# Performance work log

Measured on AMD Instinct MI355X. Metric: run time of the kernel, lower is better.

Reference implementation:

```python
import jax, jax.numpy as jnp
import numpy as np

N_NODES = 100000
N_EDGES = 1600000
IN_DIM = 64
HIDDEN_DIM = 64


def setup_inputs() -> dict:
    key = jax.random.key(0)
    ks = jax.random.split(key, 8)
    x = jax.random.normal(ks[0], (N_NODES, IN_DIM), dtype=jnp.float32)
    edge_index = jax.random.randint(ks[1], (2, N_EDGES), 0, N_NODES, dtype=jnp.int32)
    s = 1.0 / np.sqrt(IN_DIM)
    sh = 1.0 / np.sqrt(HIDDEN_DIM)
    # SAGEConv params: lin_l (applied to mean-aggregated neighbors, with bias),
    # lin_r (applied to root/self features, no bias) -- PyG defaults.
    w1l = jax.random.uniform(ks[2], (IN_DIM, HIDDEN_DIM), jnp.float32, -s, s)
    b1l = jax.random.uniform(ks[3], (HIDDEN_DIM,), jnp.float32, -s, s)
    w1r = jax.random.uniform(ks[4], (IN_DIM, HIDDEN_DIM), jnp.float32, -s, s)
    w2l = jax.random.uniform(ks[5], (HIDDEN_DIM, HIDDEN_DIM), jnp.float32, -sh, sh)
    b2l = jax.random.uniform(ks[6], (HIDDEN_DIM,), jnp.float32, -sh, sh)
    w2r = jax.random.uniform(ks[7], (HIDDEN_DIM, HIDDEN_DIM), jnp.float32, -sh, sh)
    return {"x": x, "edge_index": edge_index, "w1l": w1l, "b1l": b1l,
            "w1r": w1r, "w2l": w2l, "b2l": b2l, "w2r": w2r}


def reference(x, edge_index, w1l, b1l, w1r, w2l, b2l, w2r):
    n = x.shape[0]
    src, dst = edge_index[0], edge_index[1]
    # in-degree (number of incoming messages per target node), clamped to 1
    deg = jax.ops.segment_sum(jnp.ones(src.shape, x.dtype), dst, num_segments=n)
    inv_deg = 1.0 / jnp.maximum(deg, 1.0)  # [N]

    def sage_conv(h, wl, bl, wr):
        # mean aggregation of neighbor messages: scatter-add then normalize
        agg = jax.ops.segment_sum(h[src], dst, num_segments=n) * inv_deg[:, None]
        return agg @ wl + bl + h @ wr

    h = jax.nn.relu(sage_conv(x, w1l, b1l, w1r))  # conv1 + relu
    return sage_conv(h, w2l, b2l, w2r)            # conv2 (no activation)
```

## Files before the change

kernel.cpp:

```cpp
#include <hip/hip_runtime.h>
#include <hip/hip_fp16.h>


#define DIM 64
#define BN 64
#define MAXBUCK 2048
#define CHUNK 4096
#define GCAP 2048
#define WT_STRIDE 72

using f16x8 = __attribute__((ext_vector_type(8))) _Float16;
using f32x4 = __attribute__((ext_vector_type(4))) float;

__device__ inline void addh8(float* acc, float4 raw) {
    const __half2* hp = (const __half2*)&raw;
#pragma unroll
    for (int k = 0; k < 4; ++k) {
        float2 f = __half22float2(hp[k]);
        acc[2 * k]     += f.x;
        acc[2 * k + 1] += f.y;
    }
}

__global__ __launch_bounds__(256) void prehist_kernel(const int* __restrict__ dst,
                                                      int* __restrict__ ghist,
                                                      int nE, int nbuck) {
    __shared__ int hist[MAXBUCK];
    const int t = threadIdx.x;
    for (int k = t; k < nbuck; k += 256) hist[k] = 0;
    __syncthreads();
    const int base = blockIdx.x * CHUNK;
    const int end = min(nE, base + CHUNK);
    for (int i = base + t; i < end; i += 256)
        atomicAdd(&hist[dst[i] >> 6], 1);
    __syncthreads();
    for (int k = t; k < nbuck; k += 256)
        if (hist[k]) atomicAdd(&ghist[k], hist[k]);
}

__global__ __launch_bounds__(1024) void scan_kernel(const int* __restrict__ ghist,
                                                    int* __restrict__ boff,
                                                    int* __restrict__ gcur, int nbuck) {
    __shared__ int sa[2048], sb[2048];
    const int t = threadIdx.x;
    int v0 = (t < nbuck) ? ghist[t] : 0;
    int v1 = (t + 1024 < nbuck) ? ghist[t + 1024] : 0;
    sa[t] = v0; sa[t + 1024] = v1;
    __syncthreads();
    int* in = sa; int* out = sb;
    for (int d = 1; d < 2048; d <<= 1) {
        out[t] = in[t] + ((t >= d) ? in[t - d] : 0);
        int i2 = t + 1024;
        out[i2] = in[i2] + ((i2 >= d) ? in[i2 - d] : 0);
        __syncthreads();
        int* tmp = in; in = out; out = tmp;
    }
    if (t < nbuck) { int e = in[t] - v0; boff[t] = e; gcur[t] = e; }
    if (t + 1024 < nbuck) { int e = in[t + 1024] - v1; boff[t + 1024] = e; gcur[t + 1024] = e; }
    if (t == 0) boff[nbuck] = in[2047];
}

__device__ inline void load_bfrag(const float* __restrict__ H, long long nn, int lq,
                                  f16x8& b0, f16x8& b1) {
    const float* p = &H[nn * 64 + lq * 8];
    float4 u0 = *(const float4*)p;
    float4 u1 = *(const float4*)(p + 4);
    float4 u2 = *(const float4*)(p + 32);
    float4 u3 = *(const float4*)(p + 36);
    b0[0] = (_Float16)u0.x; b0[1] = (_Float16)u0.y; b0[2] = (_Float16)u0.z; b0[3] = (_Float16)u0.w;
    b0[4] = (_Float16)u1.x; b0[5] = (_Float16)u1.y; b0[6] = (_Float16)u1.z; b0[7] = (_Float16)u1.w;
    b1[0] = (_Float16)u2.x; b1[1] = (_Float16)u2.y; b1[2] = (_Float16)u2.z; b1[3] = (_Float16)u2.w;
    b1[4] = (_Float16)u3.x; b1[5] = (_Float16)u3.y; b1[6] = (_Float16)u3.z; b1[7] = (_Float16)u3.w;
}

__device__ void gemm_body(int bid, __half* wt,
                          const float* __restrict__ H,
                          const float* __restrict__ Wl, const float* __restrict__ Wr,
                          const float* __restrict__ bias,
                          __half* __restrict__ A, __half* __restrict__ Dbuf, int n) {
    const int t = threadIdx.x;
    for (int i = t; i < 4096; i += 256) {
        int k = i >> 6, m = i & 63;
        wt[(size_t)m * WT_STRIDE + k] = __float2half(Wl[i]);
        wt[(size_t)(64 + m) * WT_STRIDE + k] = __float2half(Wr[i]);
    }
    __syncthreads();
    const int lane = t & 63, wave = t >> 6;
    const int ln = lane & 15, lq = lane >> 4;
    f16x8 af[2][4][2];
#pragma unroll
    for (int mat = 0; mat < 2; ++mat)
#pragma unroll
        for (int mt = 0; mt < 4; ++mt)
#pragma unroll
            for (int ki = 0; ki < 2; ++ki)
                af[mat][mt][ki] = *(const f16x8*)&wt[(size_t)(mat * 64 + mt * 16 + ln) * WT_STRIDE
                                                     + ki * 32 + lq * 8];
    float4 bf[4];
#pragma unroll
    for (int mt = 0; mt < 4; ++mt)
        bf[mt] = *(const float4*)&bias[mt * 16 + lq * 4];

    const int base = bid * 256;
    for (int it = 0; it < 4; ++it) {
        const int node = base + it * 64 + wave * 16 + ln;
        const long long nn = (node < n) ? node : (n - 1);
        f16x8 b0, b1;
        load_bfrag(H, nn, lq, b0, b1);
        f32x4 acc[2][4];
#pragma unroll
        for (int mat = 0; mat < 2; ++mat)
#pragma unroll
            for (int mt = 0; mt < 4; ++mt) {
                f32x4 z = {0.f, 0.f, 0.f, 0.f};
                z = __builtin_amdgcn_mfma_f32_16x16x32_f16(af[mat][mt][0], b0, z, 0, 0, 0);
                z = __builtin_amdgcn_mfma_f32_16x16x32_f16(af[mat][mt][1], b1, z, 0, 0, 0);
                acc[mat][mt] = z;
            }
        if (node < n) {
#pragma unroll
            for (int mt = 0; mt < 4; ++mt) {
                union { __half2 h[2]; float2 f; } u;
                u.h[0] = __floats2half2_rn(acc[0][mt][0], acc[0][mt][1]);
                u.h[1] = __floats2half2_rn(acc[0][mt][2], acc[0][mt][3]);
                *(float2*)&A[(size_t)node * 64 + mt * 16 + lq * 4] = u.f;
                union { __half2 h[2]; float2 f; } v;
                v.h[0] = __floats2half2_rn(acc[1][mt][0] + bf[mt].x, acc[1][mt][1] + bf[mt].y);
                v.h[1] = __floats2half2_rn(acc[1][mt][2] + bf[mt].z, acc[1][mt][3] + bf[mt].w);
                *(float2*)&Dbuf[(size_t)node * 64 + mt * 16 + lq * 4] = v.f;
            }
        }
    }
}

__global__ __launch_bounds__(256) void part_gemm_kernel(const int* __restrict__ src,
                                                        const int* __restrict__ dst,
                                                        int* __restrict__ gcur,
                                                        unsigned* __restrict__ P,
                                                        int nE, int nbuck, int pb,
                                                        const float* __restrict__ H,
                                                        const float* __restrict__ Wl,
                                                        const float* __restrict__ Wr,
                                                        const float* __restrict__ bias,
                                                        __half* __restrict__ A,
                                                        __half* __restrict__ Dbuf, int n) {
    __shared__ __align__(16) unsigned short smem_u[2 * 64 * WT_STRIDE];
    if ((int)blockIdx.x < pb) {
        int* hist = (int*)smem_u;
        const int t = threadIdx.x;
        for (int k = t; k < nbuck; k += 256) hist[k] = 0;
        __syncthreads();
        const int base = blockIdx.x * CHUNK;
        const int end = min(nE, base + CHUNK);
        for (int i = base + t; i < end; i += 256)
            atomicAdd(&hist[dst[i] >> 6], 1);
        __syncthreads();
        for (int k = t; k < nbuck; k += 256) {
            int h = hist[k];
            hist[k] = h ? atomicAdd(&gcur[k], h) : 0;
        }
        __syncthreads();
        for (int i = base + t; i < end; i += 256) {
            int d = dst[i];
            int bk = d >> 6;
            int pos = atomicAdd(&hist[bk], 1);
            P[pos] = ((unsigned)src[i] << 6) | (unsigned)(d & 63);
        }
    } else {
        gemm_body(blockIdx.x - pb, (__half*)smem_u, H, Wl, Wr, bias, A, Dbuf, n);
    }
}

__global__ __launch_bounds__(256) void gather_gemm_kernel(const __half* __restrict__ A,
                                                          const __half* Din,
                                                          const int* __restrict__ boff,
                                                          const unsigned* __restrict__ P,
                                                          int* __restrict__ P2,
                                                          int* __restrict__ nstart,
                                                          const float* __restrict__ Wl,
                                                          const float* __restrict__ Wr,
                                                          const float* __restrict__ bias,
                                                          __half* __restrict__ A2,
                                                          __half* D2, int n) {
    __shared__ int hist[BN];
    __shared__ int rstart[BN];
    __shared__ int cur[BN];
    __shared__ int lsrc[GCAP];
    __shared__ __align__(16) __half wt[2 * 64 * WT_STRIDE];
    __shared__ __align__(16) __half tile[64 * WT_STRIDE];
    const int t = threadIdx.x;
    const int b = blockIdx.x;
    for (int i = t; i < 4096; i += 256) {
        int k = i >> 6, m = i & 63;
        wt[(size_t)m * WT_STRIDE + k] = __float2half(Wl[i]);
        wt[(size_t)(64 + m) * WT_STRIDE + k] = __float2half(Wr[i]);
    }
    if (t < BN) hist[t] = 0;
    __syncthreads();
    const int start = boff[b], end = boff[b + 1];
    const int nedge = end - start;
    for (int i = start + t; i < end; i += 256)
        atomicAdd(&hist[P[i] & 63], 1);
    __syncthreads();
    if (t < 64) {
        int v = hist[t];
        int s = v;
#pragma unroll
        for (int d = 1; d < 64; d <<= 1) {
            int u = __shfl_up(s, d);
            if (t >= d) s += u;
        }
        rstart[t] = s - v;
        cur[t] = s - v;
    }
    __syncthreads();
    if (t < 64) {
        int node = b * BN + t;
        if (node < n) nstart[node] = start + rstart[t];
    }
    if (b == 0 && t == 0) nstart[n] = boff[gridDim.x];
    const bool fits = (nedge <= GCAP);
    for (int i = start + t; i < end; i += 256) {
        unsigned p = P[i];
        int pos = atomicAdd(&cur[p & 63], 1);
        int v = (int)(p >> 6);
        if (fits) lsrc[pos] = v;
        P2[start + pos] = v;
    }
    __syncthreads();
    const int dg = t & 7;
    const size_t doff = (size_t)dg * 8;
    for (int pass = 0; pass < 2; ++pass) {
        const int r = pass * 32 + (t >> 3);
        const int node = b * BN + r;
        float o[8] = {0.f, 0.f, 0.f, 0.f, 0.f, 0.f, 0.f, 0.f};
        if (node < n) {
            const int c = hist[r];
            const int* sp = fits ? (lsrc + rstart[r]) : (P2 + start + rstart[r]);
            float acc[8] = {0.f, 0.f, 0.f, 0.f, 0.f, 0.f, 0.f, 0.f};
            int j = 0;
            for (; j + 4 <= c; j += 4) {
                int e0 = sp[j + 0], e1 = sp[j + 1], e2 = sp[j + 2], e3 = sp[j + 3];
                float4 r0 = *(const float4*)&A[(size_t)e0 * 64 + doff];
                float4 r1 = *(const float4*)&A[(size_t)e1 * 64 + doff];
                float4 r2 = *(const float4*)&A[(size_t)e2 * 64 + doff];
                float4 r3 = *(const float4*)&A[(size_t)e3 * 64 + doff];
                addh8(acc, r0); addh8(acc, r1); addh8(acc, r2); addh8(acc, r3);
            }
            for (; j < c; ++j) {
                float4 rr = *(const float4*)&A[(size_t)sp[j] * 64 + doff];
                addh8(acc, rr);
            }
            const float inv = 1.0f / fmaxf((float)c, 1.0f);
            float d8[8] = {0.f, 0.f, 0.f, 0.f, 0.f, 0.f, 0.f, 0.f};
            addh8(d8, *(const float4*)&Din[(size_t)node * 64 + doff]);
#pragma unroll
            for (int k = 0; k < 8; ++k)
                o[k] = fmaxf(fmaf(acc[k], inv, d8[k]), 0.f);
        }
        union { __half2 h[4]; float4 f; } u;
#pragma unroll
        for (int k = 0; k < 4; ++k)
            u.h[k] = __floats2half2_rn(o[2 * k], o[2 * k + 1]);
        *(float4*)&tile[(size_t)r * WT_STRIDE + doff] = u.f;
    }
    __syncthreads();
    const int lane = t & 63, wave = t >> 6;
    const int ln = lane & 15, lq = lane >> 4;
    f16x8 af[2][4][2];
#pragma unroll
    for (int mat = 0; mat < 2; ++mat)
#pragma unroll
        for (int mt = 0; mt < 4; ++mt)
#pragma unroll
            for (int ki = 0; ki < 2; ++ki)
                af[mat][mt][ki] = *(const f16x8*)&wt[(size_t)(mat * 64 + mt * 16 + ln) * WT_STRIDE
                                                     + ki * 32 + lq * 8];
    float4 bf[4];
#pragma unroll
    for (int mt = 0; mt < 4; ++mt)
        bf[mt] = *(const float4*)&bias[mt * 16 + lq * 4];

    const int r = wave * 16 + ln;
    f16x8 b0 = *(const f16x8*)&tile[(size_t)r * WT_STRIDE + lq * 8];
    f16x8 b1 = *(const f16x8*)&tile[(size_t)r * WT_STRIDE + 32 + lq * 8];
    f32x4 acc2[2][4];
#pragma unroll
    for (int mat = 0; mat < 2; ++mat)
#pragma unroll
        for (int mt = 0; mt < 4; ++mt) {
            f32x4 z = {0.f, 0.f, 0.f, 0.f};
            z = __builtin_amdgcn_mfma_f32_16x16x32_f16(af[mat][mt][0], b0, z, 0, 0, 0);
            z = __builtin_amdgcn_mfma_f32_16x16x32_f16(af[mat][mt][1], b1, z, 0, 0, 0);
            acc2[mat][mt] = z;
        }
    const int node = b * BN + r;
    if (node < n) {
#pragma unroll
        for (int mt = 0; mt < 4; ++mt) {
            union { __half2 h[2]; float2 f; } u;
            u.h[0] = __floats2half2_rn(acc2[0][mt][0], acc2[0][mt][1]);
            u.h[1] = __floats2half2_rn(acc2[0][mt][2], acc2[0][mt][3]);
            *(float2*)&A2[(size_t)node * 64 + mt * 16 + lq * 4] = u.f;
            union { __half2 h[2]; float2 f; } v;
            v.h[0] = __floats2half2_rn(acc2[1][mt][0] + bf[mt].x, acc2[1][mt][1] + bf[mt].y);
            v.h[1] = __floats2half2_rn(acc2[1][mt][2] + bf[mt].z, acc2[1][mt][3] + bf[mt].w);
            *(float2*)&D2[(size_t)node * 64 + mt * 16 + lq * 4] = v.f;
        }
    }
}

__global__ __launch_bounds__(256) void gather_csr_combine(const __half* __restrict__ A,
                                                          const __half* __restrict__ Dbuf,
                                                          const int* __restrict__ nstart,
                                                          const int* __restrict__ P2,
                                                          float* __restrict__ out, int n) {
    const int t = threadIdx.x;
    const int b = blockIdx.x;
    const int dg = t & 7;
    const size_t doff = (size_t)dg * 8;
    for (int pass = 0; pass < 2; ++pass) {
        const int r = pass * 32 + (t >> 3);
        const int node = b * BN + r;
        if (node >= n) continue;
        const int s0 = nstart[node];
        const int c = nstart[node + 1] - s0;
        const int* sp = P2 + s0;
        float acc[8] = {0.f, 0.f, 0.f, 0.f, 0.f, 0.f, 0.f, 0.f};
        int j = 0;
        for (; j + 4 <= c; j += 4) {
            int e0 = sp[j + 0], e1 = sp[j + 1], e2 = sp[j + 2], e3 = sp[j + 3];
            float4 r0 = *(const float4*)&A[(size_t)e0 * 64 + doff];
            float4 r1 = *(const float4*)&A[(size_t)e1 * 64 + doff];
            float4 r2 = *(const float4*)&A[(size_t)e2 * 64 + doff];
            float4 r3 = *(const float4*)&A[(size_t)e3 * 64 + doff];
            addh8(acc, r0); addh8(acc, r1); addh8(acc, r2); addh8(acc, r3);
        }
        for (; j < c; ++j) {
            float4 rr = *(const float4*)&A[(size_t)sp[j] * 64 + doff];
            addh8(acc, rr);
        }
        const float inv = 1.0f / fmaxf((float)c, 1.0f);
        float d8[8] = {0.f, 0.f, 0.f, 0.f, 0.f, 0.f, 0.f, 0.f};
        addh8(d8, *(const float4*)&Dbuf[(size_t)node * 64 + doff]);
        float o[8];
#pragma unroll
        for (int k = 0; k < 8; ++k)
            o[k] = fmaf(acc[k], inv, d8[k]);
        *(float4*)&out[(size_t)node * 64 + doff]     = make_float4(o[0], o[1], o[2], o[3]);
        *(float4*)&out[(size_t)node * 64 + doff + 4] = make_float4(o[4], o[5], o[6], o[7]);
    }
}

extern "C" void kernel_launch(void* const* d_in, const int* in_sizes, int n_in,
                              void* d_out, int out_size, void* d_ws, size_t ws_size,
                              hipStream_t stream) {
    const float* x   = (const float*)d_in[0];
    const int*   ei  = (const int*)d_in[1];
    const float* w1l = (const float*)d_in[2];
    const float* b1l = (const float*)d_in[3];
    const float* w1r = (const float*)d_in[4];
    const float* w2l = (const float*)d_in[5];
    const float* b2l = (const float*)d_in[6];
    const float* w2r = (const float*)d_in[7];
    float* out = (float*)d_out;

    const int N = in_sizes[0] / DIM;
    const int E = in_sizes[1] / 2;
    const int* src = ei;
    const int* dst = ei + E;
    const int nbuck = (N + BN - 1) / BN;
    const int pb = (E + CHUNK - 1) / CHUNK;
    const int gb = (N + 255) / 256;

    int* ghist = (int*)d_ws;
    int* boff = ghist + nbuck;
    int* gcur = boff + nbuck + 1;
    unsigned* P = (unsigned*)(gcur + nbuck);
    int* P2 = (int*)(P + E);
    int* nstart = P2 + E;
    uintptr_t ap = (uintptr_t)(nstart + N + 1);
    ap = (ap + 15) & ~(uintptr_t)15;
    __half* A  = (__half*)ap;
    __half* D  = A + (size_t)N * DIM;
    __half* A2 = D + (size_t)N * DIM;

    hipMemsetAsync(ghist, 0, nbuck * sizeof(int), stream);
    prehist_kernel<<<pb, 256, 0, stream>>>(dst, ghist, E, nbuck);
    scan_kernel<<<1, 1024, 0, stream>>>(ghist, boff, gcur, nbuck);
    part_gemm_kernel<<<pb + gb, 256, 0, stream>>>(src, dst, gcur, P, E, nbuck, pb,
                                                  x, w1l, w1r, b1l, A, D, N);

    gather_gemm_kernel<<<nbuck, 256, 0, stream>>>(A, D, boff, P, P2, nstart,
                                                  w2l, w2r, b2l, A2, D, N);

    gather_csr_combine<<<nbuck, 256, 0, stream>>>(A2, D, nstart, P2, out, N);
}
```

Baseline: 271.4 us.

## Use global atomics for bucket histogram/partition and alias gather LDS buffers

The histogram and partition passes drop per-block LDS histograms and instead issue one global atomicAdd per edge into the bucket counters, in a grid-stride loop over a fixed block count. This removes the shared-memory zeroing, block barriers and per-bucket flush, but it sends far more atomics to global memory, where hot buckets will contend. In the gather kernel, the edge-source staging array and the weight tile now share one LDS region, which allows a larger GCAP. The weights are held in registers and written to LDS only after the gather phase ends.

```diff
diff --git a/kernel.cpp b/kernel.cpp
--- a/kernel.cpp
+++ b/kernel.cpp
@@ -4,9 +4,8 @@
 
 #define DIM 64
 #define BN 64
-#define MAXBUCK 2048
-#define CHUNK 4096
-#define GCAP 2048
+#define PB 391
+#define GCAP 4096
 #define WT_STRIDE 72
 
 using f16x8 = __attribute__((ext_vector_type(8))) _Float16;
@@ -23,19 +22,11 @@
 }
 
 __global__ __launch_bounds__(256) void prehist_kernel(const int* __restrict__ dst,
-                                                      int* __restrict__ ghist,
-                                                      int nE, int nbuck) {
-    __shared__ int hist[MAXBUCK];
-    const int t = threadIdx.x;
-    for (int k = t; k < nbuck; k += 256) hist[k] = 0;
-    __syncthreads();
-    const int base = blockIdx.x * CHUNK;
-    const int end = min(nE, base + CHUNK);
-    for (int i = base + t; i < end; i += 256)
-        atomicAdd(&hist[dst[i] >> 6], 1);
-    __syncthreads();
-    for (int k = t; k < nbuck; k += 256)
-        if (hist[k]) atomicAdd(&ghist[k], hist[k]);
+                                                      int* __restrict__ ghist, int nE) {
+    const int tid = blockIdx.x * 256 + threadIdx.x;
+    const int stride = gridDim.x * 256;
+    for (int i = tid; i < nE; i += stride)
+        atomicAdd(&ghist[dst[i] >> 6], 1);
 }
 
 __global__ __launch_bounds__(1024) void scan_kernel(const int* __restrict__ ghist,
@@ -137,7 +128,7 @@
                                                         const int* __restrict__ dst,
                                                         int* __restrict__ gcur,
                                                         unsigned* __restrict__ P,
-                                                        int nE, int nbuck, int pb,
+                                                        int nE, int pb,
                                                         const float* __restrict__ H,
                                                         const float* __restrict__ Wl,
                                                         const float* __restrict__ Wr,
@@ -146,24 +137,13 @@
                                                         __half* __restrict__ Dbuf, int n) {
     __shared__ __align__(16) unsigned short smem_u[2 * 64 * WT_STRIDE];
     if ((int)blockIdx.x < pb) {
-        int* hist = (int*)smem_u;
-        const int t = threadIdx.x;
-        for (int k = t; k < nbuck; k += 256) hist[k] = 0;
-        __syncthreads();
-        const int base = blockIdx.x * CHUNK;
-        const int end = min(nE, base + CHUNK);
-        for (int i = base + t; i < end; i += 256)
-            atomicAdd(&hist[dst[i] >> 6], 1);
-        __syncthreads();
-        for (int k = t; k < nbuck; k += 256) {
-            int h = hist[k];
-            hist[k] = h ? atomicAdd(&gcur[k], h) : 0;
-        }
-        __syncthreads();
-        for (int i = base + t; i < end; i += 256) {
+        const int tid = blockIdx.x * 256 + threadIdx.x;
+        const int stride = pb * 256;
+#pragma unroll 4
+        for (int i = tid; i < nE; i += stride) {
             int d = dst[i];
             int bk = d >> 6;
-            int pos = atomicAdd(&hist[bk], 1);
+            int pos = atomicAdd(&gcur[bk], 1);
             P[pos] = ((unsigned)src[i] << 6) | (unsigned)(d & 63);
         }
     } else {
@@ -185,15 +165,17 @@
     __shared__ int hist[BN];
     __shared__ int rstart[BN];
     __shared__ int cur[BN];
-    __shared__ int lsrc[GCAP];
-    __shared__ __align__(16) __half wt[2 * 64 * WT_STRIDE];
+    __shared__ __align__(16) unsigned char uni[2 * 64 * WT_STRIDE * 2];
     __shared__ __align__(16) __half tile[64 * WT_STRIDE];
+    int* lsrc = (int*)uni;
+    __half* wt = (__half*)uni;
     const int t = threadIdx.x;
     const int b = blockIdx.x;
-    for (int i = t; i < 4096; i += 256) {
-        int k = i >> 6, m = i & 63;
-        wt[(size_t)m * WT_STRIDE + k] = __float2half(Wl[i]);
-        wt[(size_t)(64 + m) * WT_STRIDE + k] = __float2half(Wr[i]);
+    float4 wl4[4], wr4[4];
+#pragma unroll
+    for (int j = 0; j < 4; ++j) {
+        wl4[j] = ((const float4*)Wl)[j * 256 + t];
+        wr4[j] = ((const float4*)Wr)[j * 256 + t];
     }
     if (t < BN) hist[t] = 0;
     __syncthreads();
@@ -265,6 +247,17 @@
         *(float4*)&tile[(size_t)r * WT_STRIDE + doff] = u.f;
     }
     __syncthreads();
+#pragma unroll
+    for (int j = 0; j < 4; ++j) {
+#pragma unroll
+        for (int e = 0; e < 4; ++e) {
+            int i = 4 * (j * 256 + t) + e;
+            int k = i >> 6, m = i & 63;
+            wt[(size_t)m * WT_STRIDE + k] = __float2half(((const float*)&wl4[j])[e]);
+            wt[(size_t)(64 + m) * WT_STRIDE + k] = __float2half(((const float*)&wr4[j])[e]);
+        }
+    }
+    __syncthreads();
     const int lane = t & 63, wave = t >> 6;
     const int ln = lane & 15, lq = lane >> 4;
     f16x8 af[2][4][2];
@@ -370,7 +363,7 @@
     const int* src = ei;
     const int* dst = ei + E;
     const int nbuck = (N + BN - 1) / BN;
-    const int pb = (E + CHUNK - 1) / CHUNK;
+    const int pb = PB;
     const int gb = (N + 255) / 256;
 
     int* ghist = (int*)d_ws;
@@ -386,9 +379,9 @@
     __half* A2 = D + (size_t)N * DIM;
 
     hipMemsetAsync(ghist, 0, nbuck * sizeof(int), stream);
-    prehist_kernel<<<pb, 256, 0, stream>>>(dst, ghist, E, nbuck);
+    prehist_kernel<<<pb, 256, 0, stream>>>(dst, ghist, E);
     scan_kernel<<<1, 1024, 0, stream>>>(ghist, boff, gcur, nbuck);
-    part_gemm_kernel<<<pb + gb, 256, 0, stream>>>(src, dst, gcur, P, E, nbuck, pb,
+    part_gemm_kernel<<<pb + gb, 256, 0, stream>>>(src, dst, gcur, P, E, pb,
                                                   x, w1l, w1r, b1l, A, D, N);
 
     gather_gemm_kernel<<<nbuck, 256, 0, stream>>>(A, D, boff, P, P2, nstart,
```

Measured after the change: 681.6 us. 2.51x slower.
